# Kernel optimization log

Measured on AMD Instinct MI355X. Metric: run time of the kernel, lower is better.

## Reference

```python
import jax, jax.numpy as jnp
import numpy as np

LABEL_SIZE = 50
NUM_LABELS = LABEL_SIZE + 2  # + start, end
START = NUM_LABELS - 2
END = NUM_LABELS - 1
NEG = -100.0


def setup_inputs() -> dict:
    key = jax.random.key(0)
    k1, k2, k3, k4, k5 = jax.random.split(key, 5)
    B, S, D = 128, 512, 1024
    inputs = jax.random.normal(k1, (B, S, D), dtype=jnp.float32)
    lens = jax.random.randint(k2, (B,), 1, S + 1)
    labels = jax.random.randint(k3, (B, S), 0, LABEL_SIZE)
    # Linear: uniform(-bias, bias) with bias = sqrt(6/(out+in))
    bound = np.sqrt(6.0 / (LABEL_SIZE + D))
    W = jax.random.uniform(k4, (LABEL_SIZE, D), minval=-bound, maxval=bound, dtype=jnp.float32)
    b = jnp.zeros((LABEL_SIZE,), dtype=jnp.float32)
    transition = jax.random.normal(k5, (NUM_LABELS, NUM_LABELS), dtype=jnp.float32)
    # transition[to, from]; disallow from=END (column) and to=START (row)
    transition = transition.at[:, END].set(NEG)
    transition = transition.at[START, :].set(NEG)
    return {"inputs": inputs, "W": W, "b": b, "transition": transition,
            "lens": lens, "labels": labels}


def _crf_loss(inputs, W, b, transition, lens, labels):
    B, S, D = inputs.shape
    # emission scores (B, S, label_size) -> padded to (B, S, NUM_LABELS)
    logits = jnp.einsum('bsd,ld->bsl', inputs, W) + b
    logits = jnp.concatenate(
        [logits, jnp.full((B, S, 2), NEG, dtype=logits.dtype)], axis=-1)
    mask = jnp.arange(S)[None, :] < lens[:, None]  # (B, S)

    # ---- norm score: forward algorithm over time (scan) ----
    alpha0 = jnp.full((B, NUM_LABELS), NEG, dtype=logits.dtype).at[:, START].set(0.0)

    def step(alpha, xs):
        logit_t, m_t = xs  # (B, L), (B,)
        # mat[b, j, i] = alpha[b, i] + transition[j, i] + logit_t[b, j]
        mat = alpha[:, None, :] + transition[None, :, :] + logit_t[:, :, None]
        alpha_nxt = jax.nn.logsumexp(mat, axis=2)
        alpha = jnp.where(m_t[:, None], alpha_nxt, alpha)
        return alpha, None

    xs = (jnp.swapaxes(logits, 0, 1), jnp.swapaxes(mask, 0, 1))
    alpha, _ = jax.lax.scan(step, alpha0, xs)
    norm_score = jax.nn.logsumexp(alpha + transition[END][None, :], axis=1)  # (B,)

    # ---- gold score ----
    # unary: emission at gold labels
    unary = jnp.take_along_axis(logits, labels[:, :, None], axis=2)[..., 0]
    unary_score = jnp.sum(unary * mask, axis=1)
    # binary: start -> y1 -> ... -> y_len -> end
    labels_ext = jnp.concatenate(
        [jnp.full((B, 1), START, dtype=labels.dtype), labels,
         jnp.full((B, 1), END, dtype=labels.dtype)], axis=1)  # (B, S+2)
    valid = jnp.arange(S + 2)[None, :] < (lens + 1)[:, None]
    labels_ext = jnp.where(valid, labels_ext, END)
    pair = transition[labels_ext[:, 1:], labels_ext[:, :-1]]  # (B, S+1)
    pair_mask = jnp.arange(S + 1)[None, :] < (lens + 1)[:, None]
    binary_score = jnp.sum(pair * pair_mask, axis=1)

    gold_score = unary_score + binary_score
    return -jnp.sum(gold_score - norm_score)


def reference(inputs, W, b, transition, lens, labels):
    return _crf_loss(inputs, W, b, transition, lens, labels)
```

## Files before the change

### kernel.cpp

```cpp
#include <hip/hip_runtime.h>
#include <stdint.h>

#define LBL 50
#define NL 52
#define L2E 1.4426950408889634f
#define BB 128
#define SS 512
#define DD 1024

typedef __attribute__((ext_vector_type(8))) short short8;
typedef __attribute__((ext_vector_type(4))) float float4v;

union S8U { unsigned int u[4]; short8 s; };

static __device__ __forceinline__ unsigned int f2bf(float f) {
    union { float f; unsigned int u; } v; v.f = f;
    unsigned int r = v.u + 0x7fffu + ((v.u >> 16) & 1u);
    return r >> 16;
}

__global__ __launch_bounds__(256) void wconv(
    const float* __restrict__ W, unsigned short* __restrict__ Wbf)
{
    int i = blockIdx.x * 256 + threadIdx.x;
    int r = i >> 10, c = i & 1023;
    float v = (r < LBL) ? W[r * DD + c] : 0.f;
    Wbf[i] = (unsigned short)f2bf(v);
}

__global__ __launch_bounds__(256) void gemm_pe(
    const float* __restrict__ A,
    const unsigned short* __restrict__ Wbf,
    const float* __restrict__ bias,
    float* __restrict__ PEp)
{
    const int tid  = threadIdx.x;
    const int lane = tid & 63;
    const int wv   = tid >> 6;
    const int mrow = lane & 15;
    const int quad = lane >> 4;
    const int row  = blockIdx.x * 64 + wv * 16 + mrow;

    const uint4* arow = (const uint4*)(A + (size_t)row * DD);

    float4v acc[4];
#pragma unroll
    for (int i = 0; i < 4; ++i) acc[i] = (float4v){0.f, 0.f, 0.f, 0.f};

#pragma unroll 4
    for (int kc = 0; kc < DD; kc += 32) {
        uint4 u0 = arow[(kc >> 2) + quad * 2];
        uint4 u1 = arow[(kc >> 2) + quad * 2 + 1];
        S8U a;
        a.u[0] = __builtin_amdgcn_perm(u0.y, u0.x, 0x07060302u);
        a.u[1] = __builtin_amdgcn_perm(u0.w, u0.z, 0x07060302u);
        a.u[2] = __builtin_amdgcn_perm(u1.y, u1.x, 0x07060302u);
        a.u[3] = __builtin_amdgcn_perm(u1.w, u1.z, 0x07060302u);
#pragma unroll
        for (int nt = 0; nt < 4; ++nt) {
            short8 bf = *(const short8*)(Wbf + (size_t)(nt * 16 + mrow) * DD + kc + quad * 8);
            acc[nt] = __builtin_amdgcn_mfma_f32_16x16x32_bf16(a.s, bf, acc[nt], 0, 0, 0);
        }
    }
    const int r0 = blockIdx.x * 64 + wv * 16 + quad * 4;
#pragma unroll
    for (int nt = 0; nt < 4; ++nt) {
        int col = nt * 16 + mrow;
        float bv = (col < LBL) ? bias[col] : 0.f;
#pragma unroll
        for (int rr = 0; rr < 4; ++rr) {
            float val = (col < LBL) ? __builtin_amdgcn_exp2f((acc[nt][rr] + bv) * L2E) : 0.f;
            PEp[(size_t)(r0 + rr) * 64 + col] = val;
        }
    }
}

__global__ __launch_bounds__(64) void crf_seg(
    const float* __restrict__ PE,
    const float* __restrict__ T,
    const int*   __restrict__ lens,
    unsigned short* __restrict__ segm,
    int* __restrict__ segc)
{
    const int sk   = blockIdx.x;
    const int s    = sk >> 4;
    const int k    = sk & 15;
    const int lane = threadIdx.x & 63;
    const int b    = lane & 15;
    const int q    = lane >> 4;
    const int L    = lens[s];
    const int t0   = 1 + k * 32;
    int tend = t0 + 31; if (L - 1 < tend) tend = L - 1;

    short8 afr[4][2];
#pragma unroll
    for (int it = 0; it < 4; ++it) {
        int i = (b >> 2) * 8 + (b & 3) + 4 * (it & 1) + 32 * (it >> 1);
#pragma unroll
        for (int jt = 0; jt < 2; ++jt) {
            S8U pk;
#pragma unroll
            for (int h = 0; h < 4; ++h) {
                int k0 = jt * 32 + q * 8 + 2 * h;
                float v0 = (i < NL && k0     < NL) ? __builtin_amdgcn_exp2f(T[i * NL + k0]     * L2E) : 0.f;
                float v1 = (i < NL && k0 + 1 < NL) ? __builtin_amdgcn_exp2f(T[i * NL + k0 + 1] * L2E) : 0.f;
                pk.u[h] = f2bf(v0) | (f2bf(v1) << 16);
            }
            afr[it][jt] = pk.s;
        }
    }

    S8U bfr[4][2];
#pragma unroll
    for (int nt = 0; nt < 4; ++nt)
#pragma unroll
        for (int kc = 0; kc < 2; ++kc)
#pragma unroll
            for (int u = 0; u < 4; ++u) {
                int kk = kc * 32 + q * 8 + 2 * u;
                int n  = nt * 16 + b;
                unsigned int v = 0;
                if (kk == n)     v |= 0x3F80u;
                if (kk + 1 == n) v |= (0x3F80u << 16);
                bfr[nt][kc].u[u] = v;
            }

    int csum = 0;
    if (t0 <= tend) {
        const float* prow = PE + (size_t)(s * SS + t0) * 64 + q * 8;
        float4 f0 = *(const float4*)(prow);
        float4 f1 = *(const float4*)(prow + 4);
        float4 f2 = *(const float4*)(prow + 32);
        float4 f3 = *(const float4*)(prow + 36);
        for (int t = t0; t <= tend; ++t) {
            const float* pn = prow + 64;
            float4 g0 = *(const float4*)(pn);
            float4 g1 = *(const float4*)(pn + 4);
            float4 g2 = *(const float4*)(pn + 32);
            float4 g3 = *(const float4*)(pn + 36);

            const float4v zz = (float4v){0.f, 0.f, 0.f, 0.f};
            float4v acc[4][4];
#pragma unroll
            for (int it = 0; it < 4; ++it)
#pragma unroll
                for (int nt = 0; nt < 4; ++nt)
                    acc[it][nt] = __builtin_amdgcn_mfma_f32_16x16x32_bf16(afr[it][0], bfr[nt][0].s, zz, 0, 0, 0);
#pragma unroll
            for (int it = 0; it < 4; ++it)
#pragma unroll
                for (int nt = 0; nt < 4; ++nt)
                    acc[it][nt] = __builtin_amdgcn_mfma_f32_16x16x32_bf16(afr[it][1], bfr[nt][1].s, acc[it][nt], 0, 0, 0);

            int myeb = (int)((__float_as_uint(acc[0][0][0]) >> 23) & 0xffu);
            int eb   = __builtin_amdgcn_readfirstlane(myeb);
            float ss = __uint_as_float((unsigned int)(254 - eb) << 23);
            csum += 127 - eb;

            float pvs[16];
            pvs[0]  = f0.x * ss; pvs[1]  = f0.y * ss; pvs[2]  = f0.z * ss; pvs[3]  = f0.w * ss;
            pvs[4]  = f1.x * ss; pvs[5]  = f1.y * ss; pvs[6]  = f1.z * ss; pvs[7]  = f1.w * ss;
            pvs[8]  = f2.x * ss; pvs[9]  = f2.y * ss; pvs[10] = f2.z * ss; pvs[11] = f2.w * ss;
            pvs[12] = f3.x * ss; pvs[13] = f3.y * ss; pvs[14] = f3.z * ss; pvs[15] = f3.w * ss;

#pragma unroll
            for (int nt = 0; nt < 4; ++nt) {
                float ev[16];
#pragma unroll
                for (int kp = 0; kp < 16; ++kp)
                    ev[kp] = acc[kp >> 2][nt][kp & 3] * pvs[kp];
#pragma unroll
                for (int kc = 0; kc < 2; ++kc)
#pragma unroll
                    for (int u = 0; u < 4; ++u)
                        bfr[nt][kc].u[u] = __builtin_amdgcn_perm(
                            __float_as_uint(ev[kc * 8 + 2 * u + 1]),
                            __float_as_uint(ev[kc * 8 + 2 * u]), 0x07060302u);
            }

            f0 = g0; f1 = g1; f2 = g2; f3 = g3;
            prow = pn;
        }
    }

    unsigned short* ob = segm + (size_t)sk * 4096;
#pragma unroll
    for (int nt = 0; nt < 4; ++nt)
#pragma unroll
        for (int kc = 0; kc < 2; ++kc) {
            uint4 st; st.x = bfr[nt][kc].u[0]; st.y = bfr[nt][kc].u[1];
            st.z = bfr[nt][kc].u[2]; st.w = bfr[nt][kc].u[3];
            *(uint4*)(ob + (nt * 16 + b) * 64 + kc * 32 + q * 8) = st;
        }
    if (lane == 0) segc[sk] = csum;
}

__global__ __launch_bounds__(128) void crf_comb(
    const float* __restrict__ PE,
    const float* __restrict__ T,
    const int*   __restrict__ lens,
    const int*   __restrict__ labels,
    const unsigned short* __restrict__ segm,
    const int*   __restrict__ segc,
    float* __restrict__ out)
{
    const int s    = blockIdx.x;
    const int tid  = threadIdx.x;
    const int lane = tid & 63;
    const int wv   = tid >> 6;

    __shared__ float gold_sh;
    float norm_ln = 0.f;

    if (wv == 1) {
        const int len = lens[s];
        const size_t base = (size_t)s * SS;
        float un2 = 0.f, bi = 0.f;
        for (int t = lane; t < len; t += 64) {
            int lab  = labels[base + t];
            int prev = (t == 0) ? LBL : labels[base + t - 1];
            un2 += __builtin_amdgcn_logf(PE[(base + t) * 64 + lab]);
            bi  += T[lab * NL + prev];
        }
        float g = un2 * (1.0f / L2E) + bi;
        g += __shfl_xor(g, 1, 64);
        g += __shfl_xor(g, 2, 64);
        g += __shfl_xor(g, 4, 64);
        g += __shfl_xor(g, 8, 64);
        g += __shfl_xor(g, 16, 64);
        g += __shfl_xor(g, 32, 64);
        if (lane == 0) {
            g += T[(NL - 1) * NL + labels[base + len - 1]];
            gold_sh = g;
        }
    } else {
        const int b = lane & 15, q = lane >> 4;
        const float4v zz = (float4v){0.f, 0.f, 0.f, 0.f};

        S8U aw[2];
#pragma unroll
        for (int kc = 0; kc < 2; ++kc)
#pragma unroll
            for (int u = 0; u < 4; ++u) {
                int j0 = kc * 32 + q * 8 + 2 * u;
                float v0 = (j0     < NL) ? __builtin_amdgcn_exp2f(T[(NL - 1) * NL + j0]     * L2E) : 0.f;
                float v1 = (j0 + 1 < NL) ? __builtin_amdgcn_exp2f(T[(NL - 1) * NL + j0 + 1] * L2E) : 0.f;
                aw[kc].u[u] = f2bf(v0) | (f2bf(v1) << 16);
            }

        int F = 0;
        float sv0 = 0.f, sv1 = 0.f, sv2 = 0.f, sv3 = 0.f;

        for (int kk = 15; kk >= 0; --kk) {
            const unsigned short* mb = segm + (size_t)(s * 16 + kk) * 4096;
            S8U bfr[4][2];
#pragma unroll
            for (int nt = 0; nt < 4; ++nt)
#pragma unroll
                for (int kc = 0; kc < 2; ++kc) {
                    uint4 ld = *(const uint4*)(mb + (nt * 16 + b) * 64 + kc * 32 + q * 8);
                    bfr[nt][kc].u[0] = ld.x; bfr[nt][kc].u[1] = ld.y;
                    bfr[nt][kc].u[2] = ld.z; bfr[nt][kc].u[3] = ld.w;
                }
            float4v acc[4];
#pragma unroll
            for (int nt = 0; nt < 4; ++nt)
                acc[nt] = __builtin_amdgcn_mfma_f32_16x16x32_bf16(aw[0].s, bfr[nt][0].s, zz, 0, 0, 0);
#pragma unroll
            for (int nt = 0; nt < 4; ++nt)
                acc[nt] = __builtin_amdgcn_mfma_f32_16x16x32_bf16(aw[1].s, bfr[nt][1].s, acc[nt], 0, 0, 0);

            int myeb = (int)((__float_as_uint(acc[0][0]) >> 23) & 0xffu);
            int eb   = __builtin_amdgcn_readfirstlane(myeb);
            float ssc = __uint_as_float((unsigned int)(254 - eb) << 23);
            F += segc[s * 16 + kk] + (127 - eb);

            sv0 = acc[0][0] * ssc; sv1 = acc[1][0] * ssc;
            sv2 = acc[2][0] * ssc; sv3 = acc[3][0] * ssc;

            if (kk == 0) break;

            float svq = (q & 2) ? ((q & 1) ? sv3 : sv2) : ((q & 1) ? sv1 : sv0);
            int svqi = __float_as_int(svq);
#pragma unroll
            for (int kc = 0; kc < 2; ++kc)
#pragma unroll
                for (int u = 0; u < 4; ++u) {
                    int j0 = kc * 32 + q * 8 + 2 * u;
                    int w0i = __builtin_amdgcn_ds_bpermute(j0 * 4,       svqi);
                    int w1i = __builtin_amdgcn_ds_bpermute((j0 + 1) * 4, svqi);
                    aw[kc].u[u] = __builtin_amdgcn_perm((unsigned)w1i, (unsigned)w0i, 0x07060302u);
                }
        }

        float dp = 0.f;
        const float* pe0 = PE + (size_t)s * SS * 64;
        float svs[4] = {sv0, sv1, sv2, sv3};
#pragma unroll
        for (int nt = 0; nt < 4; ++nt) {
            int n = nt * 16 + b;
            float e1 = (n < NL) ? pe0[n] * __builtin_amdgcn_exp2f(T[n * NL + LBL] * L2E) : 0.f;
            dp += svs[nt] * e1;
        }
        dp += __shfl_xor(dp, 1, 64);
        dp += __shfl_xor(dp, 2, 64);
        dp += __shfl_xor(dp, 4, 64);
        dp += __shfl_xor(dp, 8, 64);
        norm_ln = (__builtin_amdgcn_logf(dp) - (float)F) * (1.0f / L2E);
    }

    __syncthreads();
    if (tid == 0) atomicAdd(out, norm_ln - gold_sh);
}

extern "C" void kernel_launch(void* const* d_in, const int* in_sizes, int n_in,
                              void* d_out, int out_size, void* d_ws, size_t ws_size,
                              hipStream_t stream) {
    const float* A      = (const float*)d_in[0];
    const float* W      = (const float*)d_in[1];
    const float* bias   = (const float*)d_in[2];
    const float* T      = (const float*)d_in[3];
    const int*   lens   = (const int*)d_in[4];
    const int*   labels = (const int*)d_in[5];
    float* out = (float*)d_out;

    float* PEp = (float*)d_ws;
    unsigned short* Wbf  = (unsigned short*)((char*)d_ws + (size_t)65536 * 64 * 4);
    unsigned short* segm = (unsigned short*)((char*)d_ws + ((size_t)32 << 20));
    int*            segc = (int*)((char*)d_ws + ((size_t)56 << 20));

    hipMemsetAsync(d_out, 0, sizeof(float), stream);
    wconv<<<dim3(256), dim3(256), 0, stream>>>(W, Wbf);
    gemm_pe<<<dim3((BB * SS) / 64), dim3(256), 0, stream>>>(A, Wbf, bias, PEp);
    crf_seg<<<dim3(2048), dim3(64), 0, stream>>>(PEp, T, lens, segm, segc);
    crf_comb<<<dim3(128), dim3(128), 0, stream>>>(PEp, T, lens, labels, segm, segc, out);
}
```

Baseline: 442.3 us.

## Split segment matrix columns across four waves and double-buffer combine loads

crf_seg now runs four waves per block, and each wave owns one 16-column slice of the 64x64 segment transfer product. That cuts the per-wave MFMA chain from 32 to 8 per timestep and quarters the register state. Because each column slice now gets its own exponent scale, crf_comb reads four per-column scale counters, realigns them with a wave-wide max and split exponent multipliers, and double-buffers the segment loads so they overlap the sequential folds. In exchange there is more scale bookkeeping and a small risk to numerical range.

```diff
diff --git a/kernel.cpp b/kernel.cpp
--- a/kernel.cpp
+++ b/kernel.cpp
@@ -75,7 +75,7 @@
     }
 }
 
-__global__ __launch_bounds__(64) void crf_seg(
+__global__ __launch_bounds__(256, 4) void crf_seg(
     const float* __restrict__ PE,
     const float* __restrict__ T,
     const int*   __restrict__ lens,
@@ -85,7 +85,9 @@
     const int sk   = blockIdx.x;
     const int s    = sk >> 4;
     const int k    = sk & 15;
-    const int lane = threadIdx.x & 63;
+    const int tid  = threadIdx.x;
+    const int lane = tid & 63;
+    const int c    = tid >> 6;
     const int b    = lane & 15;
     const int q    = lane >> 4;
     const int L    = lens[s];
@@ -110,89 +112,70 @@
         }
     }
 
-    S8U bfr[4][2];
-#pragma unroll
-    for (int nt = 0; nt < 4; ++nt)
-#pragma unroll
-        for (int kc = 0; kc < 2; ++kc)
-#pragma unroll
-            for (int u = 0; u < 4; ++u) {
-                int kk = kc * 32 + q * 8 + 2 * u;
-                int n  = nt * 16 + b;
-                unsigned int v = 0;
-                if (kk == n)     v |= 0x3F80u;
-                if (kk + 1 == n) v |= (0x3F80u << 16);
-                bfr[nt][kc].u[u] = v;
-            }
+    S8U bfr[2];
+#pragma unroll
+    for (int kc = 0; kc < 2; ++kc)
+#pragma unroll
+        for (int u = 0; u < 4; ++u) {
+            int kk = kc * 32 + q * 8 + 2 * u;
+            int n  = c * 16 + b;
+            unsigned int v = 0;
+            if (kk == n)     v |= 0x3F80u;
+            if (kk + 1 == n) v |= (0x3F80u << 16);
+            bfr[kc].u[u] = v;
+        }
 
     int csum = 0;
-    if (t0 <= tend) {
-        const float* prow = PE + (size_t)(s * SS + t0) * 64 + q * 8;
+    const float* prow = PE + (size_t)(s * SS + t0) * 64 + q * 8;
+    for (int t = t0; t <= tend; ++t) {
         float4 f0 = *(const float4*)(prow);
         float4 f1 = *(const float4*)(prow + 4);
         float4 f2 = *(const float4*)(prow + 32);
         float4 f3 = *(const float4*)(prow + 36);
-        for (int t = t0; t <= tend; ++t) {
-            const float* pn = prow + 64;
-            float4 g0 = *(const float4*)(pn);
-            float4 g1 = *(const float4*)(pn + 4);
-            float4 g2 = *(const float4*)(pn + 32);
-            float4 g3 = *(const float4*)(pn + 36);
-
-            const float4v zz = (float4v){0.f, 0.f, 0.f, 0.f};
-            float4v acc[4][4];
-#pragma unroll
-            for (int it = 0; it < 4; ++it)
-#pragma unroll
-                for (int nt = 0; nt < 4; ++nt)
-                    acc[it][nt] = __builtin_amdgcn_mfma_f32_16x16x32_bf16(afr[it][0], bfr[nt][0].s, zz, 0, 0, 0);
-#pragma unroll
-            for (int it = 0; it < 4; ++it)
-#pragma unroll
-                for (int nt = 0; nt < 4; ++nt)
-                    acc[it][nt] = __builtin_amdgcn_mfma_f32_16x16x32_bf16(afr[it][1], bfr[nt][1].s, acc[it][nt], 0, 0, 0);
-
-            int myeb = (int)((__float_as_uint(acc[0][0][0]) >> 23) & 0xffu);
-            int eb   = __builtin_amdgcn_readfirstlane(myeb);
-            float ss = __uint_as_float((unsigned int)(254 - eb) << 23);
-            csum += 127 - eb;
-
-            float pvs[16];
-            pvs[0]  = f0.x * ss; pvs[1]  = f0.y * ss; pvs[2]  = f0.z * ss; pvs[3]  = f0.w * ss;
-            pvs[4]  = f1.x * ss; pvs[5]  = f1.y * ss; pvs[6]  = f1.z * ss; pvs[7]  = f1.w * ss;
-            pvs[8]  = f2.x * ss; pvs[9]  = f2.y * ss; pvs[10] = f2.z * ss; pvs[11] = f2.w * ss;
-            pvs[12] = f3.x * ss; pvs[13] = f3.y * ss; pvs[14] = f3.z * ss; pvs[15] = f3.w * ss;
-
-#pragma unroll
-            for (int nt = 0; nt < 4; ++nt) {
-                float ev[16];
-#pragma unroll
-                for (int kp = 0; kp < 16; ++kp)
-                    ev[kp] = acc[kp >> 2][nt][kp & 3] * pvs[kp];
-#pragma unroll
-                for (int kc = 0; kc < 2; ++kc)
-#pragma unroll
-                    for (int u = 0; u < 4; ++u)
-                        bfr[nt][kc].u[u] = __builtin_amdgcn_perm(
-                            __float_as_uint(ev[kc * 8 + 2 * u + 1]),
-                            __float_as_uint(ev[kc * 8 + 2 * u]), 0x07060302u);
-            }
-
-            f0 = g0; f1 = g1; f2 = g2; f3 = g3;
-            prow = pn;
-        }
+
+        const float4v zz = (float4v){0.f, 0.f, 0.f, 0.f};
+        float4v acc[4];
+#pragma unroll
+        for (int it = 0; it < 4; ++it)
+            acc[it] = __builtin_amdgcn_mfma_f32_16x16x32_bf16(afr[it][0], bfr[0].s, zz, 0, 0, 0);
+#pragma unroll
+        for (int it = 0; it < 4; ++it)
+            acc[it] = __builtin_amdgcn_mfma_f32_16x16x32_bf16(afr[it][1], bfr[1].s, acc[it], 0, 0, 0);
+
+        int myeb = (int)((__float_as_uint(acc[0][0]) >> 23) & 0xffu);
+        int eb   = __builtin_amdgcn_readfirstlane(myeb);
+        float ss = __uint_as_float((unsigned int)(254 - eb) << 23);
+        csum += 127 - eb;
+
+        float pvs[16];
+        pvs[0]  = f0.x * ss; pvs[1]  = f0.y * ss; pvs[2]  = f0.z * ss; pvs[3]  = f0.w * ss;
+        pvs[4]  = f1.x * ss; pvs[5]  = f1.y * ss; pvs[6]  = f1.z * ss; pvs[7]  = f1.w * ss;
+        pvs[8]  = f2.x * ss; pvs[9]  = f2.y * ss; pvs[10] = f2.z * ss; pvs[11] = f2.w * ss;
+        pvs[12] = f3.x * ss; pvs[13] = f3.y * ss; pvs[14] = f3.z * ss; pvs[15] = f3.w * ss;
+
+        float ev[16];
+#pragma unroll
+        for (int kp = 0; kp < 16; ++kp)
+            ev[kp] = acc[kp >> 2][kp & 3] * pvs[kp];
+#pragma unroll
+        for (int kc = 0; kc < 2; ++kc)
+#pragma unroll
+            for (int u = 0; u < 4; ++u)
+                bfr[kc].u[u] = __builtin_amdgcn_perm(
+                    __float_as_uint(ev[kc * 8 + 2 * u + 1]),
+                    __float_as_uint(ev[kc * 8 + 2 * u]), 0x07060302u);
+
+        prow += 64;
     }
 
     unsigned short* ob = segm + (size_t)sk * 4096;
 #pragma unroll
-    for (int nt = 0; nt < 4; ++nt)
-#pragma unroll
-        for (int kc = 0; kc < 2; ++kc) {
-            uint4 st; st.x = bfr[nt][kc].u[0]; st.y = bfr[nt][kc].u[1];
-            st.z = bfr[nt][kc].u[2]; st.w = bfr[nt][kc].u[3];
-            *(uint4*)(ob + (nt * 16 + b) * 64 + kc * 32 + q * 8) = st;
-        }
-    if (lane == 0) segc[sk] = csum;
+    for (int kc = 0; kc < 2; ++kc) {
+        uint4 st; st.x = bfr[kc].u[0]; st.y = bfr[kc].u[1];
+        st.z = bfr[kc].u[2]; st.w = bfr[kc].u[3];
+        *(uint4*)(ob + (c * 16 + b) * 64 + kc * 32 + q * 8) = st;
+    }
+    if (lane == 0) segc[sk * 4 + c] = csum;
 }
 
 __global__ __launch_bounds__(128) void crf_comb(
@@ -248,65 +231,98 @@
                 aw[kc].u[u] = f2bf(v0) | (f2bf(v1) << 16);
             }
 
-        int F = 0;
-        float sv0 = 0.f, sv1 = 0.f, sv2 = 0.f, sv3 = 0.f;
-
-        for (int kk = 15; kk >= 0; --kk) {
-            const unsigned short* mb = segm + (size_t)(s * 16 + kk) * 4096;
-            S8U bfr[4][2];
-#pragma unroll
-            for (int nt = 0; nt < 4; ++nt)
-#pragma unroll
-                for (int kc = 0; kc < 2; ++kc) {
-                    uint4 ld = *(const uint4*)(mb + (nt * 16 + b) * 64 + kc * 32 + q * 8);
-                    bfr[nt][kc].u[0] = ld.x; bfr[nt][kc].u[1] = ld.y;
-                    bfr[nt][kc].u[2] = ld.z; bfr[nt][kc].u[3] = ld.w;
-                }
-            float4v acc[4];
-#pragma unroll
-            for (int nt = 0; nt < 4; ++nt)
-                acc[nt] = __builtin_amdgcn_mfma_f32_16x16x32_bf16(aw[0].s, bfr[nt][0].s, zz, 0, 0, 0);
-#pragma unroll
-            for (int nt = 0; nt < 4; ++nt)
-                acc[nt] = __builtin_amdgcn_mfma_f32_16x16x32_bf16(aw[1].s, bfr[nt][1].s, acc[nt], 0, 0, 0);
-
-            int myeb = (int)((__float_as_uint(acc[0][0]) >> 23) & 0xffu);
-            int eb   = __builtin_amdgcn_readfirstlane(myeb);
-            float ssc = __uint_as_float((unsigned int)(254 - eb) << 23);
-            F += segc[s * 16 + kk] + (127 - eb);
-
-            sv0 = acc[0][0] * ssc; sv1 = acc[1][0] * ssc;
-            sv2 = acc[2][0] * ssc; sv3 = acc[3][0] * ssc;
-
-            if (kk == 0) break;
-
-            float svq = (q & 2) ? ((q & 1) ? sv3 : sv2) : ((q & 1) ? sv1 : sv0);
-            int svqi = __float_as_int(svq);
-#pragma unroll
-            for (int kc = 0; kc < 2; ++kc)
-#pragma unroll
-                for (int u = 0; u < 4; ++u) {
-                    int j0 = kc * 32 + q * 8 + 2 * u;
-                    int w0i = __builtin_amdgcn_ds_bpermute(j0 * 4,       svqi);
-                    int w1i = __builtin_amdgcn_ds_bpermute((j0 + 1) * 4, svqi);
-                    aw[kc].u[u] = __builtin_amdgcn_perm((unsigned)w1i, (unsigned)w0i, 0x07060302u);
-                }
-        }
+        int Fw = 0;
+        float sv[4] = {0.f, 0.f, 0.f, 0.f};
+
+        S8U bufA[4][2], bufB[4][2];
+        int scA[4], scB[4];
+
+#define LOADSEG(BUF, SC, KK) do {                                                 \
+        const unsigned short* mb = segm + (size_t)(s * 16 + (KK)) * 4096;         \
+        _Pragma("unroll")                                                         \
+        for (int nt = 0; nt < 4; ++nt)                                            \
+            _Pragma("unroll")                                                     \
+            for (int kc = 0; kc < 2; ++kc) {                                      \
+                uint4 ld = *(const uint4*)(mb + (nt * 16 + b) * 64 + kc * 32 + q * 8); \
+                BUF[nt][kc].u[0] = ld.x; BUF[nt][kc].u[1] = ld.y;                 \
+                BUF[nt][kc].u[2] = ld.z; BUF[nt][kc].u[3] = ld.w;                 \
+            }                                                                     \
+        int4 s4 = *(const int4*)(segc + (s * 16 + (KK)) * 4);                     \
+        SC[0] = s4.x; SC[1] = s4.y; SC[2] = s4.z; SC[3] = s4.w;                   \
+    } while (0)
+
+#define FOLD(BUF, SC, KK) do {                                                    \
+        float4v acc[4];                                                           \
+        _Pragma("unroll")                                                         \
+        for (int nt = 0; nt < 4; ++nt)                                            \
+            acc[nt] = __builtin_amdgcn_mfma_f32_16x16x32_bf16(aw[0].s, BUF[nt][0].s, zz, 0, 0, 0); \
+        _Pragma("unroll")                                                         \
+        for (int nt = 0; nt < 4; ++nt)                                            \
+            acc[nt] = __builtin_amdgcn_mfma_f32_16x16x32_bf16(aw[1].s, BUF[nt][1].s, acc[nt], 0, 0, 0); \
+        int mm[4], te[4];                                                         \
+        _Pragma("unroll")                                                         \
+        for (int nt = 0; nt < 4; ++nt) {                                          \
+            mm[nt] = Fw + SC[nt];                                                 \
+            unsigned bt = __float_as_uint(acc[nt][0]);                            \
+            int ebf = (int)((bt >> 23) & 255u);                                   \
+            te[nt] = (acc[nt][0] == 0.f) ? (int)0xC1000000 : (ebf - 127 - mm[nt]);\
+        }                                                                         \
+        int tm = te[0]; tm = (te[1] > tm) ? te[1] : tm;                           \
+        tm = (te[2] > tm) ? te[2] : tm; tm = (te[3] > tm) ? te[3] : tm;           \
+        tm = max(tm, __shfl_xor(tm, 1, 64));                                      \
+        tm = max(tm, __shfl_xor(tm, 2, 64));                                      \
+        tm = max(tm, __shfl_xor(tm, 4, 64));                                      \
+        tm = max(tm, __shfl_xor(tm, 8, 64));                                      \
+        int Fnew = -tm;                                                           \
+        _Pragma("unroll")                                                         \
+        for (int nt = 0; nt < 4; ++nt) {                                          \
+            int e_m = Fnew - mm[nt];                                              \
+            int h1 = e_m >> 1; int h2 = e_m - h1;                                 \
+            float m1 = __uint_as_float((unsigned)(h1 + 127) << 23);               \
+            float m2 = __uint_as_float((unsigned)(h2 + 127) << 23);               \
+            sv[nt] = (e_m < -252) ? 0.f : acc[nt][0] * m1 * m2;                   \
+        }                                                                         \
+        Fw = Fnew;                                                                \
+        if ((KK) > 0) {                                                           \
+            float svq = (q & 2) ? ((q & 1) ? sv[3] : sv[2])                       \
+                                : ((q & 1) ? sv[1] : sv[0]);                      \
+            int svqi = __float_as_int(svq);                                       \
+            _Pragma("unroll")                                                     \
+            for (int kc = 0; kc < 2; ++kc)                                        \
+                _Pragma("unroll")                                                 \
+                for (int u = 0; u < 4; ++u) {                                     \
+                    int j0 = kc * 32 + q * 8 + 2 * u;                             \
+                    int w0i = __builtin_amdgcn_ds_bpermute(j0 * 4,       svqi);   \
+                    int w1i = __builtin_amdgcn_ds_bpermute((j0 + 1) * 4, svqi);   \
+                    aw[kc].u[u] = __builtin_amdgcn_perm((unsigned)w1i, (unsigned)w0i, 0x07060302u); \
+                }                                                                 \
+        }                                                                         \
+    } while (0)
+
+        LOADSEG(bufA, scA, 15);
+        for (int kp = 0; kp < 8; ++kp) {
+            int kk = 15 - 2 * kp;
+            if (kk >= 1) LOADSEG(bufB, scB, kk - 1);
+            FOLD(bufA, scA, kk);
+            if (kk >= 2) LOADSEG(bufA, scA, kk - 2);
+            FOLD(bufB, scB, kk - 1);
+        }
+#undef FOLD
+#undef LOADSEG
 
         float dp = 0.f;
         const float* pe0 = PE + (size_t)s * SS * 64;
-        float svs[4] = {sv0, sv1, sv2, sv3};
 #pragma unroll
         for (int nt = 0; nt < 4; ++nt) {
             int n = nt * 16 + b;
             float e1 = (n < NL) ? pe0[n] * __builtin_amdgcn_exp2f(T[n * NL + LBL] * L2E) : 0.f;
-            dp += svs[nt] * e1;
+            dp += sv[nt] * e1;
         }
         dp += __shfl_xor(dp, 1, 64);
         dp += __shfl_xor(dp, 2, 64);
         dp += __shfl_xor(dp, 4, 64);
         dp += __shfl_xor(dp, 8, 64);
-        norm_ln = (__builtin_amdgcn_logf(dp) - (float)F) * (1.0f / L2E);
+        norm_ln = (__builtin_amdgcn_logf(dp) - (float)Fw) * (1.0f / L2E);
     }
 
     __syncthreads();
@@ -332,6 +348,6 @@
     hipMemsetAsync(d_out, 0, sizeof(float), stream);
     wconv<<<dim3(256), dim3(256), 0, stream>>>(W, Wbf);
     gemm_pe<<<dim3((BB * SS) / 64), dim3(256), 0, stream>>>(A, Wbf, bias, PEp);
-    crf_seg<<<dim3(2048), dim3(64), 0, stream>>>(PEp, T, lens, segm, segc);
+    crf_seg<<<dim3(2048), dim3(256), 0, stream>>>(PEp, T, lens, segm, segc);
     crf_comb<<<dim3(128), dim3(128), 0, stream>>>(PEp, T, lens, labels, segm, segc, out);
 }
```

New measurement: 471.8 us. 1.07x slower.
